# Kernel optimization log

Measured on AMD Instinct MI355X. Metric: run time of the kernel, lower is better.

## Reference

```python
import jax, jax.numpy as jnp
import numpy as np

EPS = 1e-5
LEAK = 0.33  # scn LeakyReLU default leakiness


def leaky(x):
    return jnp.where(x > 0, x, LEAK * x)


def subm_conv(feat, idx, mask, w):
    # feat: [N,C], idx: [N,K] int, mask: [N,K] bool, w: [K,Cin,Cout]
    g = feat[idx] * mask[..., None]          # [N,K,C] gather of active neighbors
    return jnp.einsum('nkc,kcd->nd', g, w)   # [N,Cout]


def batch_norm(x, gamma, beta):
    # scn BatchNormalization in training mode: batch stats over active sites
    m = x.mean(axis=0)
    v = x.var(axis=0)
    return (x - m) * jax.lax.rsqrt(v + EPS) * gamma + beta


def setup_inputs() -> dict:
    key = jax.random.key(0)
    ks = jax.random.split(key, 8)
    N, K, C, B = 131072, 9, 64, 4
    features = jax.random.normal(ks[0], (N, C), dtype=jnp.float32)
    neighbor_idx = jax.random.randint(ks[1], (N, K), 0, N, dtype=jnp.int32)
    # center offset always points at self (submanifold conv semantics)
    neighbor_idx = neighbor_idx.at[:, K // 2].set(jnp.arange(N, dtype=jnp.int32))
    neighbor_mask = jax.random.randint(ks[2], (N, K), 0, 2) > 0
    neighbor_mask = neighbor_mask.at[:, K // 2].set(True)
    scale = 1.0 / np.sqrt(K * C)
    conv1_w = jax.random.normal(ks[3], (B, K, C, C), dtype=jnp.float32) * scale
    conv2_w = jax.random.normal(ks[4], (B, K, C, C), dtype=jnp.float32) * scale
    bn1_gamma = jnp.ones((B, C), dtype=jnp.float32)
    bn1_beta = jnp.zeros((B, C), dtype=jnp.float32)
    bn2_gamma = jnp.ones((B, C), dtype=jnp.float32)
    bn2_beta = jnp.zeros((B, C), dtype=jnp.float32)
    return {
        'features': features, 'neighbor_idx': neighbor_idx, 'neighbor_mask': neighbor_mask,
        'conv1_w': conv1_w, 'bn1_gamma': bn1_gamma, 'bn1_beta': bn1_beta,
        'conv2_w': conv2_w, 'bn2_gamma': bn2_gamma, 'bn2_beta': bn2_beta,
    }


def reference(features, neighbor_idx, neighbor_mask, conv1_w, bn1_gamma, bn1_beta,
              conv2_w, bn2_gamma, bn2_beta):
    x = features
    n_blocks = conv1_w.shape[0]
    for b in range(n_blocks):
        residual = x
        out = subm_conv(x, neighbor_idx, neighbor_mask, conv1_w[b])
        out = leaky(batch_norm(out, bn1_gamma[b], bn1_beta[b]))
        out = subm_conv(out, neighbor_idx, neighbor_mask, conv2_w[b])
        out = batch_norm(out, bn2_gamma[b], bn2_beta[b])
        x = leaky(out + residual)
    return x
```

## Files before the change

### kernel.cpp

```cpp
#include <hip/hip_runtime.h>
#include <hip/hip_bf16.h>
#include <stdint.h>

#define NROWS 131072
#define EPSBN 1e-5f
#define LEAKK 0.33f
#define NCOPY 8

typedef __bf16 bf16x8_t __attribute__((ext_vector_type(8)));
typedef float  f32x4_t  __attribute__((ext_vector_type(4)));

__device__ __forceinline__ float leaky_f(float x) { return fmaxf(x, LEAKK * x); }

#define GLDS16(g, l)                                                          \
    __builtin_amdgcn_global_load_lds(                                         \
        (const __attribute__((address_space(1))) void*)(g),                   \
        (__attribute__((address_space(3))) void*)(l), 16, 0, 0)

#define CFENCE() asm volatile("" ::: "memory")


__global__ __launch_bounds__(256, 4) void conv_kernel(
    const __bf16* __restrict__ src,
    const int* __restrict__ cidxT,
    const __bf16* __restrict__ wt,
    __bf16* __restrict__ dst,
    float* __restrict__ stat_out)
{
    __shared__ char Bw[2][8192];

    const int tid  = threadIdx.x;
    const int lane = tid & 63;
    const int wv   = tid >> 6;
    const int quad = lane >> 4;
    const int l15  = lane & 15;
    const int row0 = blockIdx.x << 7;
    const int srow = tid >> 3;
    const int cg   = (tid & 7) ^ (srow & 7);
    const int ldsl = (tid & 192) << 4;
    const int sxor = l15 & 7;

    const char* srcb = (const char*)src;
    const char* wtb  = (const char*)wt;

    f32x4_t acc[2][4];
#pragma unroll
    for (int mt = 0; mt < 2; ++mt)
#pragma unroll
        for (int nt = 0; nt < 4; ++nt)
            acc[mt][nt] = (f32x4_t){0.f, 0.f, 0.f, 0.f};

    const int ibase = row0 + (wv << 5) + l15;
    const unsigned qofs = (unsigned)(quad << 4);

    int ixv[2][2];
#pragma unroll
    for (int mt = 0; mt < 2; ++mt) ixv[0][mt] = cidxT[ibase + (mt << 4)];
#pragma unroll
    for (int mt = 0; mt < 2; ++mt) ixv[1][mt] = cidxT[NROWS + ibase + (mt << 4)];
    CFENCE();
#pragma unroll
    for (int i = 0; i < 2; ++i)
        GLDS16(wtb + (((i << 5) + srow) << 7) + (cg << 4),
               &Bw[0][(i << 12) + ldsl]);
    CFENCE();
    bf16x8_t areg[2][2][2];
#pragma unroll
    for (int mt = 0; mt < 2; ++mt) {
        unsigned vo = ((unsigned)ixv[0][mt] << 7) + qofs;
#pragma unroll
        for (int ks = 0; ks < 2; ++ks)
            areg[0][mt][ks] = *(const bf16x8_t*)(srcb + vo + (ks << 6));
    }
    CFENCE();

#pragma unroll
    for (int k = 0; k < 9; ++k) {
        if (k < 7) {
#pragma unroll
            for (int mt = 0; mt < 2; ++mt)
                ixv[k & 1][mt] = cidxT[(k + 2) * NROWS + ibase + (mt << 4)];
        }
        CFENCE();
        if (k < 8) {
#pragma unroll
            for (int i = 0; i < 2; ++i)
                GLDS16(wtb + ((size_t)(k + 1) << 13)
                           + (((i << 5) + srow) << 7) + (cg << 4),
                       &Bw[(k + 1) & 1][(i << 12) + ldsl]);
        }
        CFENCE();
        if (k < 8) {
#pragma unroll
            for (int mt = 0; mt < 2; ++mt) {
                unsigned vo = ((unsigned)ixv[(k + 1) & 1][mt] << 7) + qofs;
#pragma unroll
                for (int ks = 0; ks < 2; ++ks)
                    areg[(k + 1) & 1][mt][ks] =
                        *(const bf16x8_t*)(srcb + vo + (ks << 6));
            }
        }
        CFENCE();
        if (k < 7)       asm volatile("s_waitcnt vmcnt(12)" ::: "memory");
        else if (k == 7) asm volatile("s_waitcnt vmcnt(10)" ::: "memory");
        else             asm volatile("s_waitcnt vmcnt(4)"  ::: "memory");
        __builtin_amdgcn_s_barrier();
        bf16x8_t bq[4][2];
#pragma unroll
        for (int ks = 0; ks < 2; ++ks) {
            const int slot = ((quad | (ks << 2)) ^ sxor) << 4;
#pragma unroll
            for (int nt = 0; nt < 4; ++nt)
                bq[nt][ks] = *(const bf16x8_t*)
                    &Bw[k & 1][(((nt << 4) + l15) << 7) + slot];
        }
        __builtin_amdgcn_s_setprio(1);
#pragma unroll
        for (int ks = 0; ks < 2; ++ks)
#pragma unroll
            for (int mt = 0; mt < 2; ++mt)
#pragma unroll
                for (int nt = 0; nt < 4; ++nt)
                    acc[mt][nt] = __builtin_amdgcn_mfma_f32_16x16x32_bf16(
                        areg[k & 1][mt][ks], bq[nt][ks], acc[mt][nt], 0, 0, 0);
        __builtin_amdgcn_s_setprio(0);
        CFENCE();
        asm volatile("s_waitcnt lgkmcnt(0)" ::: "memory");
        __builtin_amdgcn_s_barrier();
        CFENCE();
    }

#pragma unroll
    for (int mt = 0; mt < 2; ++mt) {
        int rowb = row0 + (wv << 5) + (mt << 4) + (quad << 2);
#pragma unroll
        for (int nt = 0; nt < 4; ++nt) {
            int col = (nt << 4) + l15;
#pragma unroll
            for (int r = 0; r < 4; ++r)
                dst[((size_t)(rowb + r) << 6) + col] = (__bf16)acc[mt][nt][r];
        }
    }
    float* red = (float*)Bw;
    __syncthreads();
    if (tid < 128) red[tid] = 0.f;
    __syncthreads();
#pragma unroll
    for (int nt = 0; nt < 4; ++nt) {
        float s = 0.f, q = 0.f;
#pragma unroll
        for (int mt = 0; mt < 2; ++mt)
#pragma unroll
            for (int r = 0; r < 4; ++r) { float v = acc[mt][nt][r]; s += v; q += v * v; }
        s += __shfl_xor(s, 16); s += __shfl_xor(s, 32);
        q += __shfl_xor(q, 16); q += __shfl_xor(q, 32);
        if (lane < 16) {
            atomicAdd(&red[(nt << 4) + lane], s);
            atomicAdd(&red[64 + (nt << 4) + lane], q);
        }
    }
    __syncthreads();
    if (tid < 128)
        atomicAdd(&stat_out[((blockIdx.x & (NCOPY - 1)) << 7) + tid], red[tid]);
}

__global__ __launch_bounds__(256, 4) void convbn_kernel(
    const __bf16* __restrict__ src,
    const int* __restrict__ cidxT,
    const __bf16* __restrict__ wt,
    __bf16* __restrict__ dst,
    float* __restrict__ stat_out,
    const float* __restrict__ stat_in,
    const float* __restrict__ gamma, const float* __restrict__ beta)
{
    __shared__ char Bw[2][8192];
    __shared__ float scsh[128];
    __shared__ float scD[64], shD[64];

    const int tid  = threadIdx.x;
    const int lane = tid & 63;
    const int wv   = tid >> 6;
    const int quad = lane >> 4;
    const int l15  = lane & 15;
    const int row0 = blockIdx.x << 7;
    const int srow = tid >> 3;
    const int cg   = (tid & 7) ^ (srow & 7);
    const int ldsl = (tid & 192) << 4;
    const int sxor = l15 & 7;

    const char* srcb = (const char*)src;
    const char* wtb  = (const char*)wt;

    f32x4_t acc[2][4];
#pragma unroll
    for (int mt = 0; mt < 2; ++mt)
#pragma unroll
        for (int nt = 0; nt < 4; ++nt)
            acc[mt][nt] = (f32x4_t){0.f, 0.f, 0.f, 0.f};

    const int ibase = row0 + (wv << 5) + l15;
    const unsigned qofs = (unsigned)(quad << 4);

    int ixv[2][2], ixs[2][2];
#pragma unroll
    for (int mt = 0; mt < 2; ++mt) ixv[0][mt] = cidxT[ibase + (mt << 4)];
#pragma unroll
    for (int mt = 0; mt < 2; ++mt) ixv[1][mt] = cidxT[NROWS + ibase + (mt << 4)];
    CFENCE();
#pragma unroll
    for (int i = 0; i < 2; ++i)
        GLDS16(wtb + (((i << 5) + srow) << 7) + (cg << 4),
               &Bw[0][(i << 12) + ldsl]);
    CFENCE();
    if (tid < 128) {
        float s = 0.f;
#pragma unroll
        for (int c = 0; c < NCOPY; ++c) s += stat_in[(c << 7) + tid];
        scsh[tid] = s;
    }
    __syncthreads();
    if (tid < 64) {
        float m = scsh[tid] * (1.f / NROWS);
        float v = scsh[64 + tid] * (1.f / NROWS) - m * m;
        float s = gamma[tid] * rsqrtf(v + EPSBN);
        scD[tid] = s;
        shD[tid] = beta[tid] - m * s;
    }
    __syncthreads();
    asm volatile("s_waitcnt vmcnt(0)" ::: "memory");
    __builtin_amdgcn_s_barrier();
    CFENCE();

    bf16x8_t areg[2][2][2];
#pragma unroll
    for (int mt = 0; mt < 2; ++mt) {
        ixs[0][mt] = ixv[0][mt];
        unsigned vo = ((unsigned)ixv[0][mt] << 7) + qofs;
#pragma unroll
        for (int ks = 0; ks < 2; ++ks)
            areg[0][mt][ks] = *(const bf16x8_t*)(srcb + vo + (ks << 6));
    }
    CFENCE();

#pragma unroll
    for (int k = 0; k < 9; ++k) {
        if (k < 7) {
#pragma unroll
            for (int mt = 0; mt < 2; ++mt)
                ixv[k & 1][mt] = cidxT[(k + 2) * NROWS + ibase + (mt << 4)];
        }
        CFENCE();
        if (k < 8) {
#pragma unroll
            for (int i = 0; i < 2; ++i)
                GLDS16(wtb + ((size_t)(k + 1) << 13)
                           + (((i << 5) + srow) << 7) + (cg << 4),
                       &Bw[(k + 1) & 1][(i << 12) + ldsl]);
        }
        CFENCE();
        if (k < 8) {
#pragma unroll
            for (int mt = 0; mt < 2; ++mt) {
                int ix = ixv[(k + 1) & 1][mt];
                ixs[(k + 1) & 1][mt] = ix;
                unsigned vo = ((unsigned)ix << 7) + qofs;
#pragma unroll
                for (int ks = 0; ks < 2; ++ks)
                    areg[(k + 1) & 1][mt][ks] =
                        *(const bf16x8_t*)(srcb + vo + (ks << 6));
            }
        }
        CFENCE();
        if (k < 7)       asm volatile("s_waitcnt vmcnt(12)" ::: "memory");
        else if (k == 7) asm volatile("s_waitcnt vmcnt(10)" ::: "memory");
        else             asm volatile("s_waitcnt vmcnt(4)"  ::: "memory");
        __builtin_amdgcn_s_barrier();
        f32x4_t scq[2][2], shq[2][2];
#pragma unroll
        for (int ks = 0; ks < 2; ++ks) {
            int cb = (ks << 5) + (quad << 3);
            scq[ks][0] = *(const f32x4_t*)&scD[cb];
            scq[ks][1] = *(const f32x4_t*)&scD[cb + 4];
            shq[ks][0] = *(const f32x4_t*)&shD[cb];
            shq[ks][1] = *(const f32x4_t*)&shD[cb + 4];
        }
        bf16x8_t ta[2][2];
        const bf16x8_t zfrag = {};
#pragma unroll
        for (int mt = 0; mt < 2; ++mt) {
            bool dead = (ixs[k & 1][mt] == NROWS);
#pragma unroll
            for (int ks = 0; ks < 2; ++ks) {
                bf16x8_t a = areg[k & 1][mt][ks];
                bf16x8_t t;
#pragma unroll
                for (int j = 0; j < 8; ++j) {
                    float f = (float)a[j];
                    float y = fmaf(scq[ks][j >> 2][j & 3], f,
                                   shq[ks][j >> 2][j & 3]);
                    y = fmaxf(y, LEAKK * y);
                    t[j] = (__bf16)y;
                }
                ta[mt][ks] = dead ? zfrag : t;
            }
        }
        bf16x8_t bq[4][2];
#pragma unroll
        for (int ks = 0; ks < 2; ++ks) {
            const int slot = ((quad | (ks << 2)) ^ sxor) << 4;
#pragma unroll
            for (int nt = 0; nt < 4; ++nt)
                bq[nt][ks] = *(const bf16x8_t*)
                    &Bw[k & 1][(((nt << 4) + l15) << 7) + slot];
        }
        __builtin_amdgcn_s_setprio(1);
#pragma unroll
        for (int ks = 0; ks < 2; ++ks)
#pragma unroll
            for (int mt = 0; mt < 2; ++mt)
#pragma unroll
                for (int nt = 0; nt < 4; ++nt)
                    acc[mt][nt] = __builtin_amdgcn_mfma_f32_16x16x32_bf16(
                        ta[mt][ks], bq[nt][ks], acc[mt][nt], 0, 0, 0);
        __builtin_amdgcn_s_setprio(0);
        CFENCE();
        asm volatile("s_waitcnt lgkmcnt(0)" ::: "memory");
        __builtin_amdgcn_s_barrier();
        CFENCE();
    }

#pragma unroll
    for (int mt = 0; mt < 2; ++mt) {
        int rowb = row0 + (wv << 5) + (mt << 4) + (quad << 2);
#pragma unroll
        for (int nt = 0; nt < 4; ++nt) {
            int col = (nt << 4) + l15;
#pragma unroll
            for (int r = 0; r < 4; ++r)
                dst[((size_t)(rowb + r) << 6) + col] = (__bf16)acc[mt][nt][r];
        }
    }
    float* red = (float*)Bw;
    __syncthreads();
    if (tid < 128) red[tid] = 0.f;
    __syncthreads();
#pragma unroll
    for (int nt = 0; nt < 4; ++nt) {
        float s = 0.f, q = 0.f;
#pragma unroll
        for (int mt = 0; mt < 2; ++mt)
#pragma unroll
            for (int r = 0; r < 4; ++r) { float v = acc[mt][nt][r]; s += v; q += v * v; }
        s += __shfl_xor(s, 16); s += __shfl_xor(s, 32);
        q += __shfl_xor(q, 16); q += __shfl_xor(q, 32);
        if (lane < 16) {
            atomicAdd(&red[(nt << 4) + lane], s);
            atomicAdd(&red[64 + (nt << 4) + lane], q);
        }
    }
    __syncthreads();
    if (tid < 128)
        atomicAdd(&stat_out[((blockIdx.x & (NCOPY - 1)) << 7) + tid], red[tid]);
}

__global__ __launch_bounds__(256) void resid_kernel(
    const __bf16* __restrict__ z, const float* __restrict__ featin,
    __bf16* __restrict__ xh, float* __restrict__ dout,
    const float* __restrict__ stat, const float* __restrict__ gamma,
    const float* __restrict__ beta, int isfirst, int isfinal)
{
    __shared__ float sc[64], sh[64];
    int tid = threadIdx.x;
    if (tid < 128) {
        float s = 0.f;
#pragma unroll
        for (int c = 0; c < NCOPY; ++c) s += stat[(c << 7) + tid];
        if (tid < 64) sc[tid] = s;
        else          sh[tid - 64] = s;
    }
    __syncthreads();
    if (tid < 64) {
        float m = sc[tid] * (1.f / NROWS);
        float v = sh[tid] * (1.f / NROWS) - m * m;
        float s = gamma[tid] * rsqrtf(v + EPSBN);
        sc[tid] = s;
        sh[tid] = beta[tid] - m * s;
    }
    __syncthreads();
    size_t base = ((((size_t)blockIdx.x << 8) | tid) << 3);
    int c0 = (int)(base & 63);
    bf16x8_t zv = *(const bf16x8_t*)(z + base);
    float xv[8];
    if (isfirst) {
        float4 xa = *(const float4*)(featin + base);
        float4 xb = *(const float4*)(featin + base + 4);
#pragma unroll
        for (int j = 0; j < 4; ++j) { xv[j] = (&xa.x)[j]; xv[4 + j] = (&xb.x)[j]; }
    } else {
        bf16x8_t xr = *(const bf16x8_t*)(xh + base);
#pragma unroll
        for (int j = 0; j < 8; ++j) xv[j] = (float)xr[j];
    }
    float o[8];
#pragma unroll
    for (int j = 0; j < 8; ++j)
        o[j] = leaky_f((float)zv[j] * sc[c0 + j] + sh[c0 + j] + xv[j]);
    if (isfinal) {
        *(float4*)(dout + base)     = make_float4(o[0], o[1], o[2], o[3]);
        *(float4*)(dout + base + 4) = make_float4(o[4], o[5], o[6], o[7]);
    } else {
        bf16x8_t h;
#pragma unroll
        for (int j = 0; j < 8; ++j) h[j] = (__bf16)o[j];
        *(bf16x8_t*)(xh + base) = h;
    }
}

__global__ __launch_bounds__(256) void prep_kernel(
    const float* __restrict__ feat, const float* __restrict__ w1,
    const float* __restrict__ w2, const int* __restrict__ nidx,
    const unsigned char* __restrict__ mraw,
    __bf16* __restrict__ fh, __bf16* __restrict__ yh,
    __bf16* __restrict__ wtp, int* __restrict__ cidxT,
    float* __restrict__ stats)
{
    size_t t = ((size_t)blockIdx.x << 8) | threadIdx.x;
    if (t < 8192) stats[t] = 0.f;
    if (t < 64) {
        fh[(size_t)NROWS * 64 + t] = (__bf16)0.f;
        yh[(size_t)NROWS * 64 + t] = (__bf16)0.f;
    }
    if (t < 1048576) {
        size_t i = t << 3;
        float4 a = *(const float4*)(feat + i);
        float4 b = *(const float4*)(feat + i + 4);
        bf16x8_t h;
        h[0] = (__bf16)a.x; h[1] = (__bf16)a.y; h[2] = (__bf16)a.z; h[3] = (__bf16)a.w;
        h[4] = (__bf16)b.x; h[5] = (__bf16)b.y; h[6] = (__bf16)b.z; h[7] = (__bf16)b.w;
        *(bf16x8_t*)(fh + i) = h;
    }
    if (t < 294912) {
        int o = (int)t;
        int c = o & 63, d = (o >> 6) & 63;
        int kk = o >> 12;
        int k = kk % 9, bb = (kk / 9) & 3, cv = kk / 36;
        const float* w = cv ? w2 : w1;
        float v = w[((size_t)((bb * 9 + k) * 64 + c) << 6) + d];
        wtp[o] = (__bf16)v;
    }
    if (t < NROWS) {
        int n = (int)t;
        bool benc = (mraw[13] != 0);
        const unsigned int* mw = (const unsigned int*)mraw;
#pragma unroll
        for (int j = 0; j < 9; ++j) {
            int e = n * 9 + j;
            bool m = benc ? (mraw[e] != 0) : (mw[e] != 0u);
            cidxT[j * NROWS + n] = m ? nidx[e] : NROWS;
        }
    }
}

extern "C" void kernel_launch(void* const* d_in, const int* in_sizes, int n_in,
                              void* d_out, int out_size, void* d_ws, size_t ws_size,
                              hipStream_t stream) {
    const float* feat = (const float*)d_in[0];
    const int* nidx = (const int*)d_in[1];
    const unsigned char* mraw = (const unsigned char*)d_in[2];
    const float* w1 = (const float*)d_in[3];
    const float* g1 = (const float*)d_in[4];
    const float* b1 = (const float*)d_in[5];
    const float* w2 = (const float*)d_in[6];
    const float* g2 = (const float*)d_in[7];
    const float* b2 = (const float*)d_in[8];
    float* out = (float*)d_out;

    char* ws = (char*)d_ws;
    __bf16* xh    = (__bf16*)ws;
    __bf16* yh    = (__bf16*)(ws + 17825792);
    __bf16* zh    = (__bf16*)(ws + 35651584);
    __bf16* wtp   = (__bf16*)(ws + 53477376);
    float*  stats = (float*)(ws + 54525952);
    int*    cidxT = (int*)(ws + 54591488);

    prep_kernel<<<4096, 256, 0, stream>>>(feat, w1, w2, nidx, mraw,
                                          xh, yh, wtp, cidxT, stats);

    for (int b = 0; b < 4; ++b) {
        conv_kernel<<<1024, 256, 0, stream>>>(
            xh, cidxT, wtp + (size_t)b * 9 * 4096,
            yh, stats + (size_t)(2 * b) * 1024);
        convbn_kernel<<<1024, 256, 0, stream>>>(
            yh, cidxT, wtp + (size_t)(4 + b) * 9 * 4096,
            zh, stats + (size_t)(2 * b + 1) * 1024,
            stats + (size_t)(2 * b) * 1024, g1 + b * 64, b1 + b * 64);
        resid_kernel<<<4096, 256, 0, stream>>>(
            zh, feat, xh, out,
            stats + (size_t)(2 * b + 1) * 1024, g2 + b * 64, b2 + b * 64,
            (b == 0) ? 1 : 0, (b == 3) ? 1 : 0);
    }
}
```

Before: 335.6 us.

## Quantize conv1 input activations to int8 with per-row scales for gather

The first conv of each block now gathers int8-quantized neighbor rows with a per-row float scale instead of bf16 rows. The rows are dequantized to bf16 in registers before the MFMA, and the weight input channels are permuted to match the new lane layout. The resid and prep kernels now also write the int8 copy and the scales. This halves the bytes moved by the random gather, but adds dequant ALU work, an extra scale load, and int8 quantization error that compounds across blocks.

New measurement: 335.1 us. No clear change (-0.2%).

```diff
diff --git a/kernel.cpp b/kernel.cpp
--- a/kernel.cpp
+++ b/kernel.cpp
@@ -9,6 +9,7 @@
 
 typedef __bf16 bf16x8_t __attribute__((ext_vector_type(8)));
 typedef float  f32x4_t  __attribute__((ext_vector_type(4)));
+typedef int    i32x4_t  __attribute__((ext_vector_type(4)));
 
 __device__ __forceinline__ float leaky_f(float x) { return fmaxf(x, LEAKK * x); }
 
@@ -20,8 +21,25 @@
 #define CFENCE() asm volatile("" ::: "memory")
 
 
-__global__ __launch_bounds__(256, 4) void conv_kernel(
-    const __bf16* __restrict__ src,
+__device__ __forceinline__ void dequant16(i32x4_t rw, float sf,
+                                          bf16x8_t& a0, bf16x8_t& a1) {
+#pragma unroll
+    for (int d = 0; d < 4; ++d) {
+        int w = rw[d];
+#pragma unroll
+        for (int b = 0; b < 4; ++b) {
+            int v = (w << ((3 - b) << 3)) >> 24;
+            float f = (float)v * sf;
+            int j = (d << 2) + b;
+            if (j < 8) a0[j] = (__bf16)f;
+            else       a1[j & 7] = (__bf16)f;
+        }
+    }
+}
+
+__global__ __launch_bounds__(256, 4) void convq_kernel(
+    const char* __restrict__ srcq,
+    const float* __restrict__ sxa,
     const int* __restrict__ cidxT,
     const __bf16* __restrict__ wt,
     __bf16* __restrict__ dst,
@@ -40,8 +58,7 @@
     const int ldsl = (tid & 192) << 4;
     const int sxor = l15 & 7;
 
-    const char* srcb = (const char*)src;
-    const char* wtb  = (const char*)wt;
+    const char* wtb = (const char*)wt;
 
     f32x4_t acc[2][4];
 #pragma unroll
@@ -64,13 +81,13 @@
         GLDS16(wtb + (((i << 5) + srow) << 7) + (cg << 4),
                &Bw[0][(i << 12) + ldsl]);
     CFENCE();
-    bf16x8_t areg[2][2][2];
+    i32x4_t areg[2][2];
+    float   sfr[2][2];
 #pragma unroll
     for (int mt = 0; mt < 2; ++mt) {
-        unsigned vo = ((unsigned)ixv[0][mt] << 7) + qofs;
-#pragma unroll
-        for (int ks = 0; ks < 2; ++ks)
-            areg[0][mt][ks] = *(const bf16x8_t*)(srcb + vo + (ks << 6));
+        int ix = ixv[0][mt];
+        sfr[0][mt]  = sxa[ix];
+        areg[0][mt] = *(const i32x4_t*)(srcq + ((size_t)(unsigned)ix << 6) + qofs);
     }
     CFENCE();
 
@@ -93,11 +110,10 @@
         if (k < 8) {
 #pragma unroll
             for (int mt = 0; mt < 2; ++mt) {
-                unsigned vo = ((unsigned)ixv[(k + 1) & 1][mt] << 7) + qofs;
-#pragma unroll
-                for (int ks = 0; ks < 2; ++ks)
-                    areg[(k + 1) & 1][mt][ks] =
-                        *(const bf16x8_t*)(srcb + vo + (ks << 6));
+                int ix = ixv[(k + 1) & 1][mt];
+                sfr[(k + 1) & 1][mt]  = sxa[ix];
+                areg[(k + 1) & 1][mt] =
+                    *(const i32x4_t*)(srcq + ((size_t)(unsigned)ix << 6) + qofs);
             }
         }
         CFENCE();
@@ -114,6 +130,10 @@
                 bq[nt][ks] = *(const bf16x8_t*)
                     &Bw[k & 1][(((nt << 4) + l15) << 7) + slot];
         }
+        bf16x8_t ta[2][2];
+#pragma unroll
+        for (int mt = 0; mt < 2; ++mt)
+            dequant16(areg[k & 1][mt], sfr[k & 1][mt], ta[mt][0], ta[mt][1]);
         __builtin_amdgcn_s_setprio(1);
 #pragma unroll
         for (int ks = 0; ks < 2; ++ks)
@@ -122,7 +142,7 @@
 #pragma unroll
                 for (int nt = 0; nt < 4; ++nt)
                     acc[mt][nt] = __builtin_amdgcn_mfma_f32_16x16x32_bf16(
-                        areg[k & 1][mt][ks], bq[nt][ks], acc[mt][nt], 0, 0, 0);
+                        ta[mt][ks], bq[nt][ks], acc[mt][nt], 0, 0, 0);
         __builtin_amdgcn_s_setprio(0);
         CFENCE();
         asm volatile("s_waitcnt lgkmcnt(0)" ::: "memory");
@@ -365,7 +385,8 @@
 
 __global__ __launch_bounds__(256) void resid_kernel(
     const __bf16* __restrict__ z, const float* __restrict__ featin,
-    __bf16* __restrict__ xh, float* __restrict__ dout,
+    __bf16* __restrict__ xh, char* __restrict__ xq, float* __restrict__ sxa,
+    float* __restrict__ dout,
     const float* __restrict__ stat, const float* __restrict__ gamma,
     const float* __restrict__ beta, int isfirst, int isfinal)
 {
@@ -410,9 +431,22 @@
         *(float4*)(dout + base + 4) = make_float4(o[4], o[5], o[6], o[7]);
     } else {
         bf16x8_t h;
-#pragma unroll
-        for (int j = 0; j < 8; ++j) h[j] = (__bf16)o[j];
+        float mx = 1e-6f;
+#pragma unroll
+        for (int j = 0; j < 8; ++j) { h[j] = (__bf16)o[j]; mx = fmaxf(mx, fabsf(o[j])); }
+        mx = fmaxf(mx, __shfl_xor(mx, 1));
+        mx = fmaxf(mx, __shfl_xor(mx, 2));
+        mx = fmaxf(mx, __shfl_xor(mx, 4));
+        float qs = 127.f / mx;
+        unsigned long long pk = 0;
+#pragma unroll
+        for (int j = 0; j < 8; ++j) {
+            int q = (int)rintf(o[j] * qs);
+            pk |= ((unsigned long long)(unsigned char)(signed char)q) << (j << 3);
+        }
         *(bf16x8_t*)(xh + base) = h;
+        *(unsigned long long*)(xq + base) = pk;
+        if ((tid & 7) == 0) sxa[base >> 6] = mx * (1.f / 127.f);
     }
 }
 
@@ -420,33 +454,52 @@
     const float* __restrict__ feat, const float* __restrict__ w1,
     const float* __restrict__ w2, const int* __restrict__ nidx,
     const unsigned char* __restrict__ mraw,
-    __bf16* __restrict__ fh, __bf16* __restrict__ yh,
-    __bf16* __restrict__ wtp, int* __restrict__ cidxT,
-    float* __restrict__ stats)
+    __bf16* __restrict__ yh, char* __restrict__ xq, float* __restrict__ sxa,
+    __bf16* __restrict__ wtp2, __bf16* __restrict__ wtp1,
+    int* __restrict__ cidxT, float* __restrict__ stats)
 {
     size_t t = ((size_t)blockIdx.x << 8) | threadIdx.x;
     if (t < 8192) stats[t] = 0.f;
     if (t < 64) {
-        fh[(size_t)NROWS * 64 + t] = (__bf16)0.f;
         yh[(size_t)NROWS * 64 + t] = (__bf16)0.f;
+        xq[(size_t)NROWS * 64 + t] = 0;
+        if (t == 0) sxa[NROWS] = 1.f;
     }
     if (t < 1048576) {
         size_t i = t << 3;
         float4 a = *(const float4*)(feat + i);
         float4 b = *(const float4*)(feat + i + 4);
-        bf16x8_t h;
-        h[0] = (__bf16)a.x; h[1] = (__bf16)a.y; h[2] = (__bf16)a.z; h[3] = (__bf16)a.w;
-        h[4] = (__bf16)b.x; h[5] = (__bf16)b.y; h[6] = (__bf16)b.z; h[7] = (__bf16)b.w;
-        *(bf16x8_t*)(fh + i) = h;
+        float o[8] = {a.x, a.y, a.z, a.w, b.x, b.y, b.z, b.w};
+        float mx = 1e-6f;
+#pragma unroll
+        for (int j = 0; j < 8; ++j) mx = fmaxf(mx, fabsf(o[j]));
+        mx = fmaxf(mx, __shfl_xor(mx, 1));
+        mx = fmaxf(mx, __shfl_xor(mx, 2));
+        mx = fmaxf(mx, __shfl_xor(mx, 4));
+        float qs = 127.f / mx;
+        unsigned long long pk = 0;
+#pragma unroll
+        for (int j = 0; j < 8; ++j) {
+            int q = (int)rintf(o[j] * qs);
+            pk |= ((unsigned long long)(unsigned char)(signed char)q) << (j << 3);
+        }
+        *(unsigned long long*)(xq + i) = pk;
+        if ((threadIdx.x & 7) == 0) sxa[i >> 6] = mx * (1.f / 127.f);
     }
     if (t < 294912) {
         int o = (int)t;
-        int c = o & 63, d = (o >> 6) & 63;
+        int cc = o & 63, d = (o >> 6) & 63;
         int kk = o >> 12;
         int k = kk % 9, bb = (kk / 9) & 3, cv = kk / 36;
-        const float* w = cv ? w2 : w1;
-        float v = w[((size_t)((bb * 9 + k) * 64 + c) << 6) + d];
-        wtp[o] = (__bf16)v;
+        if (cv == 0) {
+            float v = w2[((size_t)((bb * 9 + k) * 64 + cc) << 6) + d];
+            wtp2[o] = (__bf16)v;
+        } else {
+            int o1 = o - 147456;
+            int ch = (cc & 7) + (((cc >> 3) & 3) << 4) + (((cc >> 5) & 1) << 3);
+            float v = w1[((size_t)((bb * 9 + k) * 64 + ch) << 6) + d];
+            wtp1[o1] = (__bf16)v;
+        }
     }
     if (t < NROWS) {
         int n = (int)t;
@@ -479,23 +532,26 @@
     __bf16* xh    = (__bf16*)ws;
     __bf16* yh    = (__bf16*)(ws + 17825792);
     __bf16* zh    = (__bf16*)(ws + 35651584);
-    __bf16* wtp   = (__bf16*)(ws + 53477376);
+    __bf16* wtp2  = (__bf16*)(ws + 53477376);
+    __bf16* wtp1  = (__bf16*)(ws + 53772288);
     float*  stats = (float*)(ws + 54525952);
     int*    cidxT = (int*)(ws + 54591488);
+    char*   xq    = ws + 59310080;
+    float*  sxa   = (float*)(ws + 67698752);
 
     prep_kernel<<<4096, 256, 0, stream>>>(feat, w1, w2, nidx, mraw,
-                                          xh, yh, wtp, cidxT, stats);
+                                          yh, xq, sxa, wtp2, wtp1, cidxT, stats);
 
     for (int b = 0; b < 4; ++b) {
-        conv_kernel<<<1024, 256, 0, stream>>>(
-            xh, cidxT, wtp + (size_t)b * 9 * 4096,
+        convq_kernel<<<1024, 256, 0, stream>>>(
+            xq, sxa, cidxT, wtp1 + (size_t)b * 36864,
             yh, stats + (size_t)(2 * b) * 1024);
         convbn_kernel<<<1024, 256, 0, stream>>>(
-            yh, cidxT, wtp + (size_t)(4 + b) * 9 * 4096,
+            yh, cidxT, wtp2 + (size_t)b * 36864,
             zh, stats + (size_t)(2 * b + 1) * 1024,
             stats + (size_t)(2 * b) * 1024, g1 + b * 64, b1 + b * 64);
         resid_kernel<<<4096, 256, 0, stream>>>(
-            zh, feat, xh, out,
+            zh, feat, xh, xq, sxa, out,
             stats + (size_t)(2 * b + 1) * 1024, g2 + b * 64, b2 + b * 64,
             (b == 0) ? 1 : 0, (b == 3) ? 1 : 0);
     }
```
